# Kernel tuning notes

Measured on AMD Instinct MI355X. Metric: run time of the kernel, lower is better.

The kernel has to match this reference:

```python
import jax, jax.numpy as jnp
import numpy as np

NUM_NODES = 10000
NUM_EDGES = 8192
NNZ = 320000
TOP_K = 5


def setup_inputs() -> dict:
    key = jax.random.key(0)
    k1, k2 = jax.random.split(key)
    # incidence list: row 0 = node ids (V_idx), row 1 = hyperedge ids (E_idx)
    edge_index = jax.random.randint(k1, (2, NNZ), 0, NUM_EDGES, dtype=jnp.int32).astype(jnp.int64)
    logits = jax.random.normal(k2, (NUM_NODES, NUM_EDGES), dtype=jnp.float32)
    return {"edge_index": edge_index, "logits": logits}


def reference(edge_index, logits):
    # Deterministic (is_test=True) path of NeuralSparseHG.forward.
    V_idx = edge_index[0]
    E_idx = edge_index[1]
    scores = jax.nn.sigmoid(logits[V_idx, E_idx])  # [nnz]

    nnz = V_idx.shape[0]
    num_nodes = logits.shape[0]

    # Segmented top-k: sort incidences by (node, -score); within each node's
    # contiguous group the first TOP_K entries are kept. This replaces the
    # original per-node Python loop with one parallel sort + rank pass.
    order = jnp.lexsort((-scores, V_idx))           # primary key V_idx asc, secondary score desc
    sorted_v = V_idx[order]
    group_start = jnp.searchsorted(sorted_v, jnp.arange(num_nodes))  # [num_nodes]
    rank_in_group = jnp.arange(nnz) - group_start[sorted_v]
    keep_sorted = rank_in_group < TOP_K

    hard_mask = jnp.zeros(nnz, scores.dtype).at[order].set(keep_sorted.astype(scores.dtype))
    # straight-through estimator (value == hard_mask, gradient == d scores)
    soft_mask = jax.lax.stop_gradient(hard_mask - scores) + scores
    keep_mask = soft_mask > 0

    # JAX cannot return data-dependent shapes under jit: instead of compacting
    # to [2, n_keep], dropped incidences are masked to -1 (same information).
    pruned_edge_index = jnp.where(keep_mask[None, :], edge_index, -1)
    return pruned_edge_index, scores
```

## Files before the change

### kernel.cpp

```cpp
#include <hip/hip_runtime.h>

#define NUM_NODES 10000
#define TOP_K 5
#define CAP 128

__global__ void k_score(const int* __restrict__ edge,
                        const float* __restrict__ logits,
                        float* __restrict__ out,
                        int* __restrict__ cnt,
                        unsigned long long* __restrict__ bucket,
                        int nnz, int num_edges) {
    int i = blockIdx.x * blockDim.x + threadIdx.x;
    if (i >= nnz) return;
    int v = edge[i];
    int e = edge[nnz + i];
    float x = logits[(long long)v * num_edges + e];
    float s = 1.0f / (1.0f + expf(-x));
    out[i]           = -1.0f;
    out[nnz + i]     = -1.0f;
    out[2 * nnz + i] = s;
    unsigned long long key =
        ((unsigned long long)__float_as_uint(s) << 32) |
        ((unsigned long long)(0x7FFFFu - (unsigned int)i) << 13) |
        (unsigned long long)(unsigned int)e;
    int pos = atomicAdd(&cnt[v], 1);
    if (pos < CAP) bucket[(long long)v * CAP + pos] = key;
}

__global__ void k_topk(const int* __restrict__ cnt,
                       const unsigned long long* __restrict__ bucket,
                       float* __restrict__ out, int nnz) {
    int wave = threadIdx.x >> 6;
    int lane = threadIdx.x & 63;
    int v = blockIdx.x * 4 + wave;
    if (v >= NUM_NODES) return;
    int n = cnt[v];
    if (n > CAP) n = CAP;
    if (n <= 0) return;

    const unsigned long long* b = bucket + (long long)v * CAP;
    unsigned long long k0 = (lane      < n) ? b[lane]      : 0ull;
    unsigned long long k1 = (lane + 64 < n) ? b[lane + 64] : 0ull;

    #pragma unroll
    for (int t = 0; t < TOP_K; t++) {
        unsigned long long m = (k0 > k1) ? k0 : k1;
        #pragma unroll
        for (int d = 32; d >= 1; d >>= 1) {
            unsigned long long o = __shfl_xor(m, d, 64);
            m = (o > m) ? o : m;
        }
        if (m == 0ull) break;
        k0 = (k0 == m) ? 0ull : k0;
        k1 = (k1 == m) ? 0ull : k1;
        if (lane == 0) {
            int e = (int)(m & 0x1FFFull);
            int i = 0x7FFFF - (int)((m >> 13) & 0x7FFFFull);
            out[i]       = (float)v;
            out[nnz + i] = (float)e;
        }
    }
}

extern "C" void kernel_launch(void* const* d_in, const int* in_sizes, int n_in,
                              void* d_out, int out_size, void* d_ws, size_t ws_size,
                              hipStream_t stream) {
    const int*   edge   = (const int*)d_in[0];
    const float* logits = (const float*)d_in[1];
    float*       out    = (float*)d_out;
    int nnz       = in_sizes[0] / 2;
    int num_edges = in_sizes[1] / NUM_NODES;

    unsigned long long* bucket = (unsigned long long*)d_ws;
    int* cnt = (int*)(bucket + (size_t)NUM_NODES * CAP);

    hipMemsetAsync(cnt, 0, NUM_NODES * sizeof(int), stream);
    k_score<<<(nnz + 255) / 256,      256, 0, stream>>>(edge, logits, out, cnt, bucket, nnz, num_edges);
    k_topk <<<(NUM_NODES + 3) / 4,    256, 0, stream>>>(cnt, bucket, out, nnz);
}
```

Baseline: 387.3 us.

## Replace per-node bucket plus wave top-k with atomicMin sorted-insert top-5 slots

Replaces the per-node 128-entry bucket, count array and wave-reduction top-k kernel with a 5-slot sorted array per node, maintained by a chain of 64-bit atomicMin insertions on inverted keys during scoring. A simple per-slot tail kernel then writes the kept incidences. This cuts the workspace footprint and the bucket read/reduce pass, and skips atomics when a score cannot enter the top-5. In exchange it adds atomic contention and a chain of up to five dependent atomics per inserting element.

After: 436.4 us. +12.7%, slower.

```diff
diff --git a/kernel.cpp b/kernel.cpp
--- a/kernel.cpp
+++ b/kernel.cpp
@@ -2,13 +2,11 @@
 
 #define NUM_NODES 10000
 #define TOP_K 5
-#define CAP 128
 
 __global__ void k_score(const int* __restrict__ edge,
                         const float* __restrict__ logits,
                         float* __restrict__ out,
-                        int* __restrict__ cnt,
-                        unsigned long long* __restrict__ bucket,
+                        unsigned long long* __restrict__ slots,
                         int nnz, int num_edges) {
     int i = blockIdx.x * blockDim.x + threadIdx.x;
     if (i >= nnz) return;
@@ -19,47 +17,37 @@
     out[i]           = -1.0f;
     out[nnz + i]     = -1.0f;
     out[2 * nnz + i] = s;
+
     unsigned long long key =
         ((unsigned long long)__float_as_uint(s) << 32) |
         ((unsigned long long)(0x7FFFFu - (unsigned int)i) << 13) |
         (unsigned long long)(unsigned int)e;
-    int pos = atomicAdd(&cnt[v], 1);
-    if (pos < CAP) bucket[(long long)v * CAP + pos] = key;
+    unsigned long long inv = ~key;
+
+    unsigned long long* sl = slots + (long long)v * TOP_K;
+    if (inv < sl[TOP_K - 1]) {
+        unsigned long long val = inv;
+        #pragma unroll
+        for (int j = 0; j < TOP_K; j++) {
+            unsigned long long old = atomicMin(&sl[j], val);
+            val = (old > val) ? old : val;
+            if (val == 0xFFFFFFFFFFFFFFFFull) break;
+        }
+    }
 }
 
-__global__ void k_topk(const int* __restrict__ cnt,
-                       const unsigned long long* __restrict__ bucket,
+__global__ void k_tail(const unsigned long long* __restrict__ slots,
                        float* __restrict__ out, int nnz) {
-    int wave = threadIdx.x >> 6;
-    int lane = threadIdx.x & 63;
-    int v = blockIdx.x * 4 + wave;
-    if (v >= NUM_NODES) return;
-    int n = cnt[v];
-    if (n > CAP) n = CAP;
-    if (n <= 0) return;
-
-    const unsigned long long* b = bucket + (long long)v * CAP;
-    unsigned long long k0 = (lane      < n) ? b[lane]      : 0ull;
-    unsigned long long k1 = (lane + 64 < n) ? b[lane + 64] : 0ull;
-
-    #pragma unroll
-    for (int t = 0; t < TOP_K; t++) {
-        unsigned long long m = (k0 > k1) ? k0 : k1;
-        #pragma unroll
-        for (int d = 32; d >= 1; d >>= 1) {
-            unsigned long long o = __shfl_xor(m, d, 64);
-            m = (o > m) ? o : m;
-        }
-        if (m == 0ull) break;
-        k0 = (k0 == m) ? 0ull : k0;
-        k1 = (k1 == m) ? 0ull : k1;
-        if (lane == 0) {
-            int e = (int)(m & 0x1FFFull);
-            int i = 0x7FFFF - (int)((m >> 13) & 0x7FFFFull);
-            out[i]       = (float)v;
-            out[nnz + i] = (float)e;
-        }
-    }
+    int t = blockIdx.x * blockDim.x + threadIdx.x;
+    if (t >= NUM_NODES * TOP_K) return;
+    unsigned long long inv = slots[t];
+    if (inv == 0xFFFFFFFFFFFFFFFFull) return;
+    unsigned long long key = ~inv;
+    int e = (int)(key & 0x1FFFull);
+    int i = 0x7FFFF - (int)((key >> 13) & 0x7FFFFull);
+    int v = t / TOP_K;
+    out[i]       = (float)v;
+    out[nnz + i] = (float)e;
 }
 
 extern "C" void kernel_launch(void* const* d_in, const int* in_sizes, int n_in,
@@ -71,10 +59,9 @@
     int nnz       = in_sizes[0] / 2;
     int num_edges = in_sizes[1] / NUM_NODES;
 
-    unsigned long long* bucket = (unsigned long long*)d_ws;
-    int* cnt = (int*)(bucket + (size_t)NUM_NODES * CAP);
+    unsigned long long* slots = (unsigned long long*)d_ws;
 
-    hipMemsetAsync(cnt, 0, NUM_NODES * sizeof(int), stream);
-    k_score<<<(nnz + 255) / 256,      256, 0, stream>>>(edge, logits, out, cnt, bucket, nnz, num_edges);
-    k_topk <<<(NUM_NODES + 3) / 4,    256, 0, stream>>>(cnt, bucket, out, nnz);
+    hipMemsetAsync(slots, 0xFF, (size_t)NUM_NODES * TOP_K * sizeof(unsigned long long), stream);
+    k_score<<<(nnz + 255) / 256,              256, 0, stream>>>(edge, logits, out, slots, nnz, num_edges);
+    k_tail <<<(NUM_NODES * TOP_K + 255) / 256, 256, 0, stream>>>(slots, out, nnz);
 }
```
